# Kernel tuning notes

Measured on AMD Instinct MI355X. Metric: run time of the kernel, lower is better.

## Reference

```python
import jax, jax.numpy as jnp
import numpy as np

B = 1024          # batch
H = 1024          # rnn_num_hidden
T = 512           # max_length (encoder timesteps)
NUM = 44          # numeric features
EMB = [(30490, 64), (7, 8), (12, 8), (3, 4)]
IN = NUM + sum(d for _, d in EMB)   # input_size = 128


def lstm_cell(x, h, c, w_ih, w_hh, b_ih, b_hh):
    # PyTorch LSTM gate order: i, f, g, o
    g = x @ w_ih.T + h @ w_hh.T + b_ih + b_hh
    i, f, gg, o = jnp.split(g, 4, axis=-1)
    c2 = jax.nn.sigmoid(f) * c + jax.nn.sigmoid(i) * jnp.tanh(gg)
    h2 = jax.nn.sigmoid(o) * jnp.tanh(c2)
    return h2, c2


def setup_inputs():
    key = jax.random.key(0)
    ks = iter(jax.random.split(key, 32))
    nrm = lambda shape, s=0.02: (s * jax.random.normal(next(ks), shape)).astype(jnp.float32)
    return {
        "x": nrm((B, 1, NUM), 1.0),
        "x_emb": jax.random.randint(next(ks), (B, 1, 4), 0, 3),
        "h0": nrm((2, B, H), 1.0),
        "c0": nrm((2, B, H), 1.0),
        "encoder_outputs": nrm((T, B, H), 1.0),
        "emb0": nrm(EMB[0]), "emb1": nrm(EMB[1]), "emb2": nrm(EMB[2]), "emb3": nrm(EMB[3]),
        "attn_w": nrm((T, IN + 2 * H)), "attn_b": nrm((T,)),
        "comb_w": nrm((IN, IN + H)), "comb_b": nrm((IN,)),
        "w_ih0": nrm((4 * H, IN)), "w_hh0": nrm((4 * H, H)),
        "b_ih0": nrm((4 * H,)), "b_hh0": nrm((4 * H,)),
        "w_ih1": nrm((4 * H, H)), "w_hh1": nrm((4 * H, H)),
        "b_ih1": nrm((4 * H,)), "b_hh1": nrm((4 * H,)),
        "pred_w": nrm((1, H)), "pred_b": nrm((1,)),
    }


def reference(x, x_emb, h0, c0, encoder_outputs, emb0, emb1, emb2, emb3,
              attn_w, attn_b, comb_w, comb_b,
              w_ih0, w_hh0, b_ih0, b_hh0, w_ih1, w_hh1, b_ih1, b_hh1,
              pred_w, pred_b):
    xt = x.transpose(1, 0, 2)[0]                       # (B, NUM)
    ids = x_emb.transpose(1, 0, 2)[0]                  # (B, 4)
    e = jnp.concatenate([emb0[ids[:, 0]], emb1[ids[:, 1]],
                         emb2[ids[:, 2]], emb3[ids[:, 3]]], axis=1)
    x_rnn = jnp.concatenate([xt, e], axis=1)           # (B, IN)
    attn_in = jnp.concatenate([x_rnn, h0[0], c0[0]], axis=1)       # (B, IN+2H)
    aw = jax.nn.softmax(attn_in @ attn_w.T + attn_b, axis=1)       # (B, T)
    ctx = jnp.einsum('bt,tbh->bh', aw, encoder_outputs)            # (B, H)
    comb = jnp.concatenate([x_rnn, ctx], axis=1) @ comb_w.T + comb_b  # (B, IN)
    h1, c1 = lstm_cell(comb, h0[0], c0[0], w_ih0, w_hh0, b_ih0, b_hh0)
    h2, c2 = lstm_cell(h1, h0[1], c0[1], w_ih1, w_hh1, b_ih1, b_hh1)
    out = h2 @ pred_w.T + pred_b                       # (B, 1)
    return out, (jnp.stack([h1, h2]), jnp.stack([c1, c2])), aw
```

## Files before the change

### kernel.cpp

```cpp
#include <hip/hip_runtime.h>
#include <hip/hip_bf16.h>

#define B 1024
#define H 1024
#define T 512
#define NUM 44
#define IN 128
#define AK (IN + 2 * H)
#define G4 (4 * H)

typedef __attribute__((ext_vector_type(8))) short s16x8;
typedef __attribute__((ext_vector_type(4))) float f32x4;

__device__ __forceinline__ unsigned short f2bf(float f) {
    unsigned u = __float_as_uint(f);
    unsigned r = (u + 0x7fffu + ((u >> 16) & 1u)) >> 16;
    return (unsigned short)r;
}

__device__ __forceinline__ void gload16(const ushort* g, ushort* l) {
    __builtin_amdgcn_global_load_lds(
        (const __attribute__((address_space(1))) void*)g,
        (__attribute__((address_space(3))) void*)l,
        16, 0, 0);
}

__global__ __launch_bounds__(256) void f32_to_bf16_kernel(
    const float* __restrict__ in, ushort* __restrict__ out, int n4)
{
    int i = blockIdx.x * 256 + threadIdx.x;
    if (i >= n4) return;
    float4 v = ((const float4*)in)[i];
    ushort4 o;
    o.x = f2bf(v.x); o.y = f2bf(v.y); o.z = f2bf(v.z); o.w = f2bf(v.w);
    ((ushort4*)out)[i] = o;
}

__global__ __launch_bounds__(256) void build_attn_in_kernel(
    const float* __restrict__ x, const int* __restrict__ x_emb,
    const float* __restrict__ h0, const float* __restrict__ c0,
    const float* __restrict__ e0, const float* __restrict__ e1,
    const float* __restrict__ e2, const float* __restrict__ e3,
    ushort* __restrict__ attn_in)
{
    int b = blockIdx.x;
    int id0 = x_emb[b * 4 + 0];
    int id1 = x_emb[b * 4 + 1];
    int id2 = x_emb[b * 4 + 2];
    int id3 = x_emb[b * 4 + 3];
    ushort* dst = attn_in + (size_t)b * AK;
    for (int j = threadIdx.x; j < AK; j += 256) {
        float v;
        if (j < 44)        v = x[b * NUM + j];
        else if (j < 108)  v = e0[id0 * 64 + (j - 44)];
        else if (j < 116)  v = e1[id1 * 8 + (j - 108)];
        else if (j < 124)  v = e2[id2 * 8 + (j - 116)];
        else if (j < 128)  v = e3[id3 * 4 + (j - 124)];
        else if (j < 1152) v = h0[b * H + (j - 128)];
        else               v = c0[b * H + (j - 1152)];
        dst[j] = f2bf(v);
    }
}

#define TM 128
#define TN 128
#define TK 32

__global__ __launch_bounds__(256) void mfma_gemm_kernel(
    const ushort* __restrict__ X1, const ushort* __restrict__ W1,
    const ushort* __restrict__ X2, const ushort* __restrict__ W2,
    const float* __restrict__ bias1, const float* __restrict__ bias2,
    float* __restrict__ Cf, ushort* __restrict__ Cb,
    int K1, int ldx1, int ldw1,
    int K2, int ldx2, int ldw2,
    int N)
{
    __shared__ ushort As[TM][TK];
    __shared__ ushort Bs[TN][TK];
    const int tid = threadIdx.x;
    const int lane = tid & 63;
    const int wid = tid >> 6;
    const int wm = wid >> 1, wn = wid & 1;
    const int m0 = blockIdx.y * TM;
    const int n0 = blockIdx.x * TN;

    const int srow = wid * 32 + (lane >> 2);
    const int skc  = (lane & 3) * 8;

    f32x4 acc[4][4] = {};

    for (int phase = 0; phase < 2; ++phase) {
        const ushort* X = phase ? X2 : X1;
        const ushort* W = phase ? W2 : W1;
        const int K   = phase ? K2 : K1;
        const int ldx = phase ? ldx2 : ldx1;
        const int ldw = phase ? ldw2 : ldw1;
        if (X == nullptr || K == 0) continue;

        for (int k0 = 0; k0 < K; k0 += TK) {
            gload16(X + (size_t)(m0 + srow) * ldx + k0 + skc,      &As[wid * 32][0]);
            gload16(X + (size_t)(m0 + srow + 16) * ldx + k0 + skc, &As[wid * 32 + 16][0]);
            gload16(W + (size_t)(n0 + srow) * ldw + k0 + skc,      &Bs[wid * 32][0]);
            gload16(W + (size_t)(n0 + srow + 16) * ldw + k0 + skc, &Bs[wid * 32 + 16][0]);
            __syncthreads();

            s16x8 a[4], b[4];
            #pragma unroll
            for (int m = 0; m < 4; ++m)
                a[m] = *(const s16x8*)&As[wm * 64 + m * 16 + (lane & 15)][(lane >> 4) * 8];
            #pragma unroll
            for (int n = 0; n < 4; ++n)
                b[n] = *(const s16x8*)&Bs[wn * 64 + n * 16 + (lane & 15)][(lane >> 4) * 8];
            #pragma unroll
            for (int m = 0; m < 4; ++m)
                #pragma unroll
                for (int n = 0; n < 4; ++n)
                    acc[m][n] = __builtin_amdgcn_mfma_f32_16x16x32_bf16(a[m], b[n], acc[m][n], 0, 0, 0);
            __syncthreads();
        }
    }

    #pragma unroll
    for (int m = 0; m < 4; ++m) {
        #pragma unroll
        for (int n = 0; n < 4; ++n) {
            int col = n0 + wn * 64 + n * 16 + (lane & 15);
            float bsum = (bias1 ? bias1[col] : 0.f) + (bias2 ? bias2[col] : 0.f);
            #pragma unroll
            for (int j = 0; j < 4; ++j) {
                int row = m0 + wm * 64 + m * 16 + (lane >> 4) * 4 + j;
                float v = acc[m][n][j] + bsum;
                if (Cf) Cf[(size_t)row * N + col] = v;
                if (Cb) Cb[(size_t)row * N + col] = f2bf(v);
            }
        }
    }
}

__global__ __launch_bounds__(256) void softmax_kernel(
    const float* __restrict__ logits, float* __restrict__ aw)
{
    int b = blockIdx.x;
    const float* row = logits + (size_t)b * T;
    int tid = threadIdx.x;
    float v0 = row[tid];
    float v1 = row[tid + 256];
    float m = fmaxf(v0, v1);
    #pragma unroll
    for (int off = 32; off > 0; off >>= 1) m = fmaxf(m, __shfl_down(m, off, 64));
    __shared__ float sm[4];
    __shared__ float ss[4];
    if ((tid & 63) == 0) sm[tid >> 6] = m;
    __syncthreads();
    m = fmaxf(fmaxf(sm[0], sm[1]), fmaxf(sm[2], sm[3]));
    float e0 = expf(v0 - m), e1 = expf(v1 - m);
    float s = e0 + e1;
    #pragma unroll
    for (int off = 32; off > 0; off >>= 1) s += __shfl_down(s, off, 64);
    if ((tid & 63) == 0) ss[tid >> 6] = s;
    __syncthreads();
    s = ss[0] + ss[1] + ss[2] + ss[3];
    float inv = 1.0f / s;
    aw[(size_t)b * T + tid]       = e0 * inv;
    aw[(size_t)b * T + tid + 256] = e1 * inv;
}

__global__ __launch_bounds__(256) void ctx_kernel(
    const float* __restrict__ enc, const float* __restrict__ aw,
    ushort* __restrict__ ctx_bf)
{
    int b = blockIdx.x;
    __shared__ float w[T];
    for (int t = threadIdx.x; t < T; t += 256) w[t] = aw[(size_t)b * T + t];
    __syncthreads();
    int h0i = threadIdx.x * 4;
    const float* p = enc + (size_t)b * H + h0i;
    float4 acc = {0.f, 0.f, 0.f, 0.f};
    #pragma unroll 8
    for (int t = 0; t < T; ++t) {
        float4 v = *(const float4*)(p + (size_t)t * B * H);
        float s = w[t];
        acc.x += s * v.x; acc.y += s * v.y; acc.z += s * v.z; acc.w += s * v.w;
    }
    ushort4 o;
    o.x = f2bf(acc.x); o.y = f2bf(acc.y); o.z = f2bf(acc.z); o.w = f2bf(acc.w);
    ((ushort4*)(ctx_bf + (size_t)b * H))[threadIdx.x] = o;
}

__device__ __forceinline__ float sigmf(float v) { return 1.0f / (1.0f + expf(-v)); }

__global__ __launch_bounds__(256) void lstm_pointwise_kernel(
    const float* __restrict__ g, const float* __restrict__ c_in,
    float* __restrict__ h_out, float* __restrict__ c_out,
    ushort* __restrict__ h_bf)
{
    int idx = blockIdx.x * 256 + threadIdx.x;
    int b = idx >> 10;
    int j = idx & 1023;
    const float* gr = g + (size_t)b * G4;
    float gi = gr[j];
    float gf = gr[j + H];
    float gc = gr[j + 2 * H];
    float go = gr[j + 3 * H];
    float c = sigmf(gf) * c_in[idx] + sigmf(gi) * tanhf(gc);
    float h = sigmf(go) * tanhf(c);
    h_out[idx] = h;
    c_out[idx] = c;
    if (h_bf) h_bf[idx] = f2bf(h);
}

__global__ __launch_bounds__(256) void pred_kernel(
    const float* __restrict__ h2, const float* __restrict__ pw,
    const float* __restrict__ pb, float* __restrict__ out)
{
    int b = blockIdx.x;
    const float* row = h2 + (size_t)b * H;
    float s = 0.f;
    for (int j = threadIdx.x; j < H; j += 256) s += row[j] * pw[j];
    #pragma unroll
    for (int off = 32; off > 0; off >>= 1) s += __shfl_down(s, off, 64);
    __shared__ float sm[4];
    if ((threadIdx.x & 63) == 0) sm[threadIdx.x >> 6] = s;
    __syncthreads();
    if (threadIdx.x == 0) out[b] = sm[0] + sm[1] + sm[2] + sm[3] + pb[0];
}

extern "C" void kernel_launch(void* const* d_in, const int* in_sizes, int n_in,
                              void* d_out, int out_size, void* d_ws, size_t ws_size,
                              hipStream_t stream) {
    (void)in_sizes; (void)n_in; (void)out_size; (void)ws_size;
    const float* x      = (const float*)d_in[0];
    const int*   x_emb  = (const int*)d_in[1];
    const float* h0     = (const float*)d_in[2];
    const float* c0     = (const float*)d_in[3];
    const float* enc    = (const float*)d_in[4];
    const float* emb0   = (const float*)d_in[5];
    const float* emb1   = (const float*)d_in[6];
    const float* emb2   = (const float*)d_in[7];
    const float* emb3   = (const float*)d_in[8];
    const float* attn_w = (const float*)d_in[9];
    const float* attn_b = (const float*)d_in[10];
    const float* comb_w = (const float*)d_in[11];
    const float* comb_b = (const float*)d_in[12];
    const float* w_ih0  = (const float*)d_in[13];
    const float* w_hh0  = (const float*)d_in[14];
    const float* b_ih0  = (const float*)d_in[15];
    const float* b_hh0  = (const float*)d_in[16];
    const float* w_ih1  = (const float*)d_in[17];
    const float* w_hh1  = (const float*)d_in[18];
    const float* b_ih1  = (const float*)d_in[19];
    const float* b_hh1  = (const float*)d_in[20];
    const float* pred_w = (const float*)d_in[21];
    const float* pred_b = (const float*)d_in[22];

    float* out = (float*)d_out;
    const size_t BH = (size_t)B * H;
    float* h1_out = out + 1024;
    float* h2_out = out + 1024 + BH;
    float* c1_out = out + 1024 + 2 * BH;
    float* c2_out = out + 1024 + 3 * BH;
    float* aw_out = out + 1024 + 4 * BH;

    char* w = (char*)d_ws;
    ushort* attn_in_bf = (ushort*)w;  w += (size_t)B * AK * 2;
    ushort* h0_bf      = (ushort*)w;  w += (size_t)2 * BH * 2;
    ushort* attn_w_bf  = (ushort*)w;  w += (size_t)T * AK * 2;
    ushort* comb_w_bf  = (ushort*)w;  w += (size_t)IN * (IN + H) * 2;
    ushort* wih0_bf    = (ushort*)w;  w += (size_t)G4 * IN * 2;
    ushort* whh0_bf    = (ushort*)w;  w += (size_t)G4 * H * 2;
    ushort* wih1_bf    = (ushort*)w;  w += (size_t)G4 * H * 2;
    ushort* whh1_bf    = (ushort*)w;  w += (size_t)G4 * H * 2;
    ushort* ctx_bf     = (ushort*)w;  w += (size_t)BH * 2;
    ushort* comb_bf    = (ushort*)w;  w += (size_t)B * IN * 2;
    ushort* h1_bf      = (ushort*)w;  w += (size_t)BH * 2;
    float*  logits     = (float*)w;   w += (size_t)B * T * 4;
    float*  g          = (float*)w;   w += (size_t)B * G4 * 4;

    #define CVT(src, dst, n) f32_to_bf16_kernel<<<((n)/4 + 255)/256, 256, 0, stream>>>(src, dst, (n)/4)
    CVT(h0,     h0_bf,     2 * B * H);
    CVT(attn_w, attn_w_bf, T * AK);
    CVT(comb_w, comb_w_bf, IN * (IN + H));
    CVT(w_ih0,  wih0_bf,   G4 * IN);
    CVT(w_hh0,  whh0_bf,   G4 * H);
    CVT(w_ih1,  wih1_bf,   G4 * H);
    CVT(w_hh1,  whh1_bf,   G4 * H);
    #undef CVT

    build_attn_in_kernel<<<B, 256, 0, stream>>>(x, x_emb, h0, c0, emb0, emb1, emb2, emb3, attn_in_bf);

    mfma_gemm_kernel<<<dim3(T / TN, B / TM), 256, 0, stream>>>(
        attn_in_bf, attn_w_bf, nullptr, nullptr, attn_b, nullptr, logits, nullptr,
        AK, AK, AK, 0, 0, 0, T);

    softmax_kernel<<<B, 256, 0, stream>>>(logits, aw_out);

    ctx_kernel<<<B, 256, 0, stream>>>(enc, aw_out, ctx_bf);

    mfma_gemm_kernel<<<dim3(IN / TN, B / TM), 256, 0, stream>>>(
        attn_in_bf, comb_w_bf, ctx_bf, comb_w_bf + IN, comb_b, nullptr, nullptr, comb_bf,
        IN, AK, IN + H, H, H, IN + H, IN);

    mfma_gemm_kernel<<<dim3(G4 / TN, B / TM), 256, 0, stream>>>(
        comb_bf, wih0_bf, h0_bf, whh0_bf, b_ih0, b_hh0, g, nullptr,
        IN, IN, IN, H, H, H, G4);

    lstm_pointwise_kernel<<<(B * H) / 256, 256, 0, stream>>>(g, c0, h1_out, c1_out, h1_bf);

    mfma_gemm_kernel<<<dim3(G4 / TN, B / TM), 256, 0, stream>>>(
        h1_bf, wih1_bf, h0_bf + BH, whh1_bf, b_ih1, b_hh1, g, nullptr,
        H, H, H, H, H, H, G4);

    lstm_pointwise_kernel<<<(B * H) / 256, 256, 0, stream>>>(g, c0 + BH, h2_out, c2_out, nullptr);

    pred_kernel<<<B, 256, 0, stream>>>(h2_out, pred_w, pred_b, out);
}
```

Baseline: 671.3 us.

## Fold comb projection into LSTM weights and fuse independent stages into megakernel

Precomputes W_ih0·comb_w and a folded bias, so layer-0 gates come from one GEMM over [x_rnn, ctx] instead of a comb GEMM followed by the input GEMM. The attention logits GEMM uses split-K with partial sums reduced inside the softmax, and softmax, context reduction and both h0·W_hh GEMMs run as independent blocks of one kernel so they overlap. Weight conversions are merged into one launch. This costs an extra 4096x1152x128 weight-product GEMM per call, extra g buffers and read-modify-write epilogues, and changes the rounding order.

```diff
diff --git a/kernel.cpp b/kernel.cpp
--- a/kernel.cpp
+++ b/kernel.cpp
@@ -7,6 +7,7 @@
 #define NUM 44
 #define IN 128
 #define AK (IN + 2 * H)
+#define XC (IN + H)
 #define G4 (4 * H)
 
 typedef __attribute__((ext_vector_type(8))) short s16x8;
@@ -25,15 +26,133 @@
         16, 0, 0);
 }
 
-__global__ __launch_bounds__(256) void f32_to_bf16_kernel(
-    const float* __restrict__ in, ushort* __restrict__ out, int n4)
+#define TM 128
+#define TN 128
+#define TK 32
+
+__device__ __forceinline__ void gemm_core(
+    const ushort* __restrict__ X, const ushort* __restrict__ W,
+    const float* __restrict__ bias1, const float* __restrict__ bias2,
+    const float* __restrict__ Cin, float* __restrict__ Cf, ushort* __restrict__ Cb,
+    int kbeg, int kend, int ldx, int ldw, int ldc,
+    int m0, int n0, ushort (*As)[TK], ushort (*Bs)[TK])
+{
+    const int tid = threadIdx.x;
+    const int lane = tid & 63;
+    const int wid = tid >> 6;
+    const int wm = wid >> 1, wn = wid & 1;
+    const int srow = wid * 32 + (lane >> 2);
+    const int skc  = (lane & 3) * 8;
+
+    f32x4 acc[4][4] = {};
+
+    for (int k0 = kbeg; k0 < kend; k0 += TK) {
+        gload16(X + (size_t)(m0 + srow) * ldx + k0 + skc,      &As[wid * 32][0]);
+        gload16(X + (size_t)(m0 + srow + 16) * ldx + k0 + skc, &As[wid * 32 + 16][0]);
+        gload16(W + (size_t)(n0 + srow) * ldw + k0 + skc,      &Bs[wid * 32][0]);
+        gload16(W + (size_t)(n0 + srow + 16) * ldw + k0 + skc, &Bs[wid * 32 + 16][0]);
+        __syncthreads();
+
+        s16x8 a[4], b[4];
+        #pragma unroll
+        for (int m = 0; m < 4; ++m)
+            a[m] = *(const s16x8*)&As[wm * 64 + m * 16 + (lane & 15)][(lane >> 4) * 8];
+        #pragma unroll
+        for (int n = 0; n < 4; ++n)
+            b[n] = *(const s16x8*)&Bs[wn * 64 + n * 16 + (lane & 15)][(lane >> 4) * 8];
+        #pragma unroll
+        for (int m = 0; m < 4; ++m)
+            #pragma unroll
+            for (int n = 0; n < 4; ++n)
+                acc[m][n] = __builtin_amdgcn_mfma_f32_16x16x32_bf16(a[m], b[n], acc[m][n], 0, 0, 0);
+        __syncthreads();
+    }
+
+    #pragma unroll
+    for (int m = 0; m < 4; ++m) {
+        #pragma unroll
+        for (int n = 0; n < 4; ++n) {
+            int col = n0 + wn * 64 + n * 16 + (lane & 15);
+            float badd = (bias1 ? bias1[col] : 0.f) + (bias2 ? bias2[col] : 0.f);
+            #pragma unroll
+            for (int j = 0; j < 4; ++j) {
+                int row = m0 + wm * 64 + m * 16 + (lane >> 4) * 4 + j;
+                float v = acc[m][n][j] + badd;
+                if (Cin) v += Cin[(size_t)row * ldc + col];
+                if (Cf) Cf[(size_t)row * ldc + col] = v;
+                if (Cb) Cb[(size_t)row * ldc + col] = f2bf(v);
+            }
+        }
+    }
+}
+
+__global__ __launch_bounds__(256) void gemm_kernel(
+    const ushort* __restrict__ X, const ushort* __restrict__ W,
+    const float* __restrict__ bias1, const float* __restrict__ bias2,
+    const float* __restrict__ Cin, float* __restrict__ Cf, ushort* __restrict__ Cb,
+    int Kchunk, int ldx, int ldw, int ldc, size_t Czstride)
+{
+    __shared__ ushort As[TM][TK];
+    __shared__ ushort Bs[TN][TK];
+    int kbeg = blockIdx.z * Kchunk;
+    gemm_core(X, W, bias1, bias2, Cin,
+              Cf ? Cf + (size_t)blockIdx.z * Czstride : nullptr, Cb,
+              kbeg, kbeg + Kchunk, ldx, ldw, ldc,
+              blockIdx.y * TM, blockIdx.x * TN, As, Bs);
+}
+
+#define CN0 524288
+#define CN1 278528
+#define CN2 131072
+#define CN3 1048576
+#define CN4 1048576
+#define CN5 1048576
+#define CNT (CN0+CN1+CN2+CN3+CN4+CN5)
+
+__global__ __launch_bounds__(256) void convert_all_kernel(
+    const float* __restrict__ s0, const float* __restrict__ s1, const float* __restrict__ s2,
+    const float* __restrict__ s3, const float* __restrict__ s4, const float* __restrict__ s5,
+    ushort* __restrict__ d0, ushort* __restrict__ d1, ushort* __restrict__ d2,
+    ushort* __restrict__ d3, ushort* __restrict__ d4, ushort* __restrict__ d5)
 {
     int i = blockIdx.x * 256 + threadIdx.x;
-    if (i >= n4) return;
-    float4 v = ((const float4*)in)[i];
+    const float* s; ushort* d;
+    if (i < CN0) { s = s0; d = d0; }
+    else if ((i -= CN0) < CN1) { s = s1; d = d1; }
+    else if ((i -= CN1) < CN2) { s = s2; d = d2; }
+    else if ((i -= CN2) < CN3) { s = s3; d = d3; }
+    else if ((i -= CN3) < CN4) { s = s4; d = d4; }
+    else if ((i -= CN4) < CN5) { s = s5; d = d5; }
+    else return;
+    float4 v = ((const float4*)s)[i];
     ushort4 o;
     o.x = f2bf(v.x); o.y = f2bf(v.y); o.z = f2bf(v.z); o.w = f2bf(v.w);
-    ((ushort4*)out)[i] = o;
+    ((ushort4*)d)[i] = o;
+}
+
+__global__ __launch_bounds__(256) void transpose_combw_kernel(
+    const float* __restrict__ comb_w, ushort* __restrict__ outT)
+{
+    int idx = blockIdx.x * 256 + threadIdx.x;
+    int j = idx >> 7;
+    int k = idx & 127;
+    outT[idx] = f2bf(comb_w[(size_t)k * XC + j]);
+}
+
+__global__ __launch_bounds__(256) void bias_f_kernel(
+    const float* __restrict__ w_ih0, const float* __restrict__ comb_b,
+    const float* __restrict__ b_ih0, const float* __restrict__ b_hh0,
+    float* __restrict__ biasf)
+{
+    __shared__ float cb[IN];
+    int i = blockIdx.x * 256 + threadIdx.x;
+    for (int j = threadIdx.x; j < IN; j += 256) cb[j] = comb_b[j];
+    __syncthreads();
+    float s = b_ih0[i] + b_hh0[i];
+    const float* row = w_ih0 + (size_t)i * IN;
+    #pragma unroll 8
+    for (int j = 0; j < IN; ++j) s += row[j] * cb[j];
+    biasf[i] = s;
 }
 
 __global__ __launch_bounds__(256) void build_attn_in_kernel(
@@ -41,7 +160,7 @@
     const float* __restrict__ h0, const float* __restrict__ c0,
     const float* __restrict__ e0, const float* __restrict__ e1,
     const float* __restrict__ e2, const float* __restrict__ e3,
-    ushort* __restrict__ attn_in)
+    ushort* __restrict__ attn_in, ushort* __restrict__ xctx)
 {
     int b = blockIdx.x;
     int id0 = x_emb[b * 4 + 0];
@@ -58,133 +177,84 @@
         else if (j < 128)  v = e3[id3 * 4 + (j - 124)];
         else if (j < 1152) v = h0[b * H + (j - 128)];
         else               v = c0[b * H + (j - 1152)];
-        dst[j] = f2bf(v);
+        unsigned short bf = f2bf(v);
+        dst[j] = bf;
+        if (j < IN) xctx[(size_t)b * XC + j] = bf;
     }
 }
 
-#define TM 128
-#define TN 128
-#define TK 32
-
-__global__ __launch_bounds__(256) void mfma_gemm_kernel(
-    const ushort* __restrict__ X1, const ushort* __restrict__ W1,
-    const ushort* __restrict__ X2, const ushort* __restrict__ W2,
-    const float* __restrict__ bias1, const float* __restrict__ bias2,
-    float* __restrict__ Cf, ushort* __restrict__ Cb,
-    int K1, int ldx1, int ldw1,
-    int K2, int ldx2, int ldw2,
-    int N)
-{
-    __shared__ ushort As[TM][TK];
-    __shared__ ushort Bs[TN][TK];
-    const int tid = threadIdx.x;
-    const int lane = tid & 63;
-    const int wid = tid >> 6;
-    const int wm = wid >> 1, wn = wid & 1;
-    const int m0 = blockIdx.y * TM;
-    const int n0 = blockIdx.x * TN;
-
-    const int srow = wid * 32 + (lane >> 2);
-    const int skc  = (lane & 3) * 8;
-
-    f32x4 acc[4][4] = {};
-
-    for (int phase = 0; phase < 2; ++phase) {
-        const ushort* X = phase ? X2 : X1;
-        const ushort* W = phase ? W2 : W1;
-        const int K   = phase ? K2 : K1;
-        const int ldx = phase ? ldx2 : ldx1;
-        const int ldw = phase ? ldw2 : ldw1;
-        if (X == nullptr || K == 0) continue;
-
-        for (int k0 = 0; k0 < K; k0 += TK) {
-            gload16(X + (size_t)(m0 + srow) * ldx + k0 + skc,      &As[wid * 32][0]);
-            gload16(X + (size_t)(m0 + srow + 16) * ldx + k0 + skc, &As[wid * 32 + 16][0]);
-            gload16(W + (size_t)(n0 + srow) * ldw + k0 + skc,      &Bs[wid * 32][0]);
-            gload16(W + (size_t)(n0 + srow + 16) * ldw + k0 + skc, &Bs[wid * 32 + 16][0]);
-            __syncthreads();
-
-            s16x8 a[4], b[4];
-            #pragma unroll
-            for (int m = 0; m < 4; ++m)
-                a[m] = *(const s16x8*)&As[wm * 64 + m * 16 + (lane & 15)][(lane >> 4) * 8];
-            #pragma unroll
-            for (int n = 0; n < 4; ++n)
-                b[n] = *(const s16x8*)&Bs[wn * 64 + n * 16 + (lane & 15)][(lane >> 4) * 8];
-            #pragma unroll
-            for (int m = 0; m < 4; ++m)
-                #pragma unroll
-                for (int n = 0; n < 4; ++n)
-                    acc[m][n] = __builtin_amdgcn_mfma_f32_16x16x32_bf16(a[m], b[n], acc[m][n], 0, 0, 0);
-            __syncthreads();
+__global__ __launch_bounds__(256) void mega_kernel(
+    const ushort* __restrict__ h0_bf, const ushort* __restrict__ whh0_bf,
+    const ushort* __restrict__ whh1_bf, float* __restrict__ g1buf, float* __restrict__ g2buf,
+    const ushort* __restrict__ wih0_bf, const ushort* __restrict__ comb_wT_bf,
+    ushort* __restrict__ W_f_bf,
+    const float* __restrict__ logits_part, const float* __restrict__ attn_b,
+    float* __restrict__ aw_out, const float* __restrict__ enc, ushort* __restrict__ xctx)
+{
+    __shared__ union {
+        struct { ushort As[TM][TK]; ushort Bs[TN][TK]; } g;
+        struct { float w[T]; float red[8]; } c;
+    } sh;
+
+    const int bid = blockIdx.x;
+    if (bid < 512) {
+        int layer = bid >> 8;
+        int t = bid & 255;
+        int m0 = (t >> 5) * TM;
+        int n0 = (t & 31) * TN;
+        gemm_core(h0_bf + (size_t)layer * B * H, layer ? whh1_bf : whh0_bf,
+                  nullptr, nullptr, nullptr, layer ? g2buf : g1buf, nullptr,
+                  0, H, H, H, G4, m0, n0, sh.g.As, sh.g.Bs);
+    } else if (bid < 800) {
+        int t = bid - 512;
+        int m0 = (t / 9) * TM;
+        int n0 = (t % 9) * TN;
+        gemm_core(wih0_bf, comb_wT_bf, nullptr, nullptr, nullptr, nullptr, W_f_bf,
+                  0, IN, IN, IN, XC, m0, n0, sh.g.As, sh.g.Bs);
+    } else {
+        int b = bid - 800;
+        int tid = threadIdx.x;
+        float v0 = attn_b[tid], v1 = attn_b[tid + 256];
+        #pragma unroll
+        for (int z = 0; z < 4; ++z) {
+            const float* lp = logits_part + (size_t)z * B * T + (size_t)b * T;
+            v0 += lp[tid];
+            v1 += lp[tid + 256];
         }
+        float m = fmaxf(v0, v1);
+        #pragma unroll
+        for (int off = 32; off > 0; off >>= 1) m = fmaxf(m, __shfl_down(m, off, 64));
+        if ((tid & 63) == 0) sh.c.red[tid >> 6] = m;
+        __syncthreads();
+        m = fmaxf(fmaxf(sh.c.red[0], sh.c.red[1]), fmaxf(sh.c.red[2], sh.c.red[3]));
+        float e0 = expf(v0 - m), e1 = expf(v1 - m);
+        float s = e0 + e1;
+        #pragma unroll
+        for (int off = 32; off > 0; off >>= 1) s += __shfl_down(s, off, 64);
+        if ((tid & 63) == 0) sh.c.red[4 + (tid >> 6)] = s;
+        __syncthreads();
+        s = sh.c.red[4] + sh.c.red[5] + sh.c.red[6] + sh.c.red[7];
+        float inv = 1.0f / s;
+        float w0 = e0 * inv, w1 = e1 * inv;
+        sh.c.w[tid] = w0;
+        sh.c.w[tid + 256] = w1;
+        aw_out[(size_t)b * T + tid]       = w0;
+        aw_out[(size_t)b * T + tid + 256] = w1;
+        __syncthreads();
+
+        int h0i = tid * 4;
+        const float* p = enc + (size_t)b * H + h0i;
+        float4 acc = {0.f, 0.f, 0.f, 0.f};
+        #pragma unroll 8
+        for (int t = 0; t < T; ++t) {
+            float4 v = *(const float4*)(p + (size_t)t * B * H);
+            float sw = sh.c.w[t];
+            acc.x += sw * v.x; acc.y += sw * v.y; acc.z += sw * v.z; acc.w += sw * v.w;
+        }
+        ushort4 o;
+        o.x = f2bf(acc.x); o.y = f2bf(acc.y); o.z = f2bf(acc.z); o.w = f2bf(acc.w);
+        *(ushort4*)(xctx + (size_t)b * XC + IN + h0i) = o;
     }
-
-    #pragma unroll
-    for (int m = 0; m < 4; ++m) {
-        #pragma unroll
-        for (int n = 0; n < 4; ++n) {
-            int col = n0 + wn * 64 + n * 16 + (lane & 15);
-            float bsum = (bias1 ? bias1[col] : 0.f) + (bias2 ? bias2[col] : 0.f);
-            #pragma unroll
-            for (int j = 0; j < 4; ++j) {
-                int row = m0 + wm * 64 + m * 16 + (lane >> 4) * 4 + j;
-                float v = acc[m][n][j] + bsum;
-                if (Cf) Cf[(size_t)row * N + col] = v;
-                if (Cb) Cb[(size_t)row * N + col] = f2bf(v);
-            }
-        }
-    }
-}
-
-__global__ __launch_bounds__(256) void softmax_kernel(
-    const float* __restrict__ logits, float* __restrict__ aw)
-{
-    int b = blockIdx.x;
-    const float* row = logits + (size_t)b * T;
-    int tid = threadIdx.x;
-    float v0 = row[tid];
-    float v1 = row[tid + 256];
-    float m = fmaxf(v0, v1);
-    #pragma unroll
-    for (int off = 32; off > 0; off >>= 1) m = fmaxf(m, __shfl_down(m, off, 64));
-    __shared__ float sm[4];
-    __shared__ float ss[4];
-    if ((tid & 63) == 0) sm[tid >> 6] = m;
-    __syncthreads();
-    m = fmaxf(fmaxf(sm[0], sm[1]), fmaxf(sm[2], sm[3]));
-    float e0 = expf(v0 - m), e1 = expf(v1 - m);
-    float s = e0 + e1;
-    #pragma unroll
-    for (int off = 32; off > 0; off >>= 1) s += __shfl_down(s, off, 64);
-    if ((tid & 63) == 0) ss[tid >> 6] = s;
-    __syncthreads();
-    s = ss[0] + ss[1] + ss[2] + ss[3];
-    float inv = 1.0f / s;
-    aw[(size_t)b * T + tid]       = e0 * inv;
-    aw[(size_t)b * T + tid + 256] = e1 * inv;
-}
-
-__global__ __launch_bounds__(256) void ctx_kernel(
-    const float* __restrict__ enc, const float* __restrict__ aw,
-    ushort* __restrict__ ctx_bf)
-{
-    int b = blockIdx.x;
-    __shared__ float w[T];
-    for (int t = threadIdx.x; t < T; t += 256) w[t] = aw[(size_t)b * T + t];
-    __syncthreads();
-    int h0i = threadIdx.x * 4;
-    const float* p = enc + (size_t)b * H + h0i;
-    float4 acc = {0.f, 0.f, 0.f, 0.f};
-    #pragma unroll 8
-    for (int t = 0; t < T; ++t) {
-        float4 v = *(const float4*)(p + (size_t)t * B * H);
-        float s = w[t];
-        acc.x += s * v.x; acc.y += s * v.y; acc.z += s * v.z; acc.w += s * v.w;
-    }
-    ushort4 o;
-    o.x = f2bf(acc.x); o.y = f2bf(acc.y); o.z = f2bf(acc.z); o.w = f2bf(acc.w);
-    ((ushort4*)(ctx_bf + (size_t)b * H))[threadIdx.x] = o;
 }
 
 __device__ __forceinline__ float sigmf(float v) { return 1.0f / (1.0f + expf(-v)); }
@@ -265,52 +335,50 @@
     ushort* attn_in_bf = (ushort*)w;  w += (size_t)B * AK * 2;
     ushort* h0_bf      = (ushort*)w;  w += (size_t)2 * BH * 2;
     ushort* attn_w_bf  = (ushort*)w;  w += (size_t)T * AK * 2;
-    ushort* comb_w_bf  = (ushort*)w;  w += (size_t)IN * (IN + H) * 2;
     ushort* wih0_bf    = (ushort*)w;  w += (size_t)G4 * IN * 2;
     ushort* whh0_bf    = (ushort*)w;  w += (size_t)G4 * H * 2;
     ushort* wih1_bf    = (ushort*)w;  w += (size_t)G4 * H * 2;
     ushort* whh1_bf    = (ushort*)w;  w += (size_t)G4 * H * 2;
-    ushort* ctx_bf     = (ushort*)w;  w += (size_t)BH * 2;
-    ushort* comb_bf    = (ushort*)w;  w += (size_t)B * IN * 2;
+    ushort* comb_wT_bf = (ushort*)w;  w += (size_t)XC * IN * 2;
+    ushort* W_f_bf     = (ushort*)w;  w += (size_t)G4 * XC * 2;
+    float*  bias_f     = (float*)w;   w += (size_t)G4 * 4;
+    ushort* xctx_bf    = (ushort*)w;  w += (size_t)B * XC * 2;
     ushort* h1_bf      = (ushort*)w;  w += (size_t)BH * 2;
-    float*  logits     = (float*)w;   w += (size_t)B * T * 4;
-    float*  g          = (float*)w;   w += (size_t)B * G4 * 4;
-
-    #define CVT(src, dst, n) f32_to_bf16_kernel<<<((n)/4 + 255)/256, 256, 0, stream>>>(src, dst, (n)/4)
-    CVT(h0,     h0_bf,     2 * B * H);
-    CVT(attn_w, attn_w_bf, T * AK);
-    CVT(comb_w, comb_w_bf, IN * (IN + H));
-    CVT(w_ih0,  wih0_bf,   G4 * IN);
-    CVT(w_hh0,  whh0_bf,   G4 * H);
-    CVT(w_ih1,  wih1_bf,   G4 * H);
-    CVT(w_hh1,  whh1_bf,   G4 * H);
-    #undef CVT
-
-    build_attn_in_kernel<<<B, 256, 0, stream>>>(x, x_emb, h0, c0, emb0, emb1, emb2, emb3, attn_in_bf);
-
-    mfma_gemm_kernel<<<dim3(T / TN, B / TM), 256, 0, stream>>>(
-        attn_in_bf, attn_w_bf, nullptr, nullptr, attn_b, nullptr, logits, nullptr,
-        AK, AK, AK, 0, 0, 0, T);
-
-    softmax_kernel<<<B, 256, 0, stream>>>(logits, aw_out);
-
-    ctx_kernel<<<B, 256, 0, stream>>>(enc, aw_out, ctx_bf);
-
-    mfma_gemm_kernel<<<dim3(IN / TN, B / TM), 256, 0, stream>>>(
-        attn_in_bf, comb_w_bf, ctx_bf, comb_w_bf + IN, comb_b, nullptr, nullptr, comb_bf,
-        IN, AK, IN + H, H, H, IN + H, IN);
-
-    mfma_gemm_kernel<<<dim3(G4 / TN, B / TM), 256, 0, stream>>>(
-        comb_bf, wih0_bf, h0_bf, whh0_bf, b_ih0, b_hh0, g, nullptr,
-        IN, IN, IN, H, H, H, G4);
-
-    lstm_pointwise_kernel<<<(B * H) / 256, 256, 0, stream>>>(g, c0, h1_out, c1_out, h1_bf);
-
-    mfma_gemm_kernel<<<dim3(G4 / TN, B / TM), 256, 0, stream>>>(
-        h1_bf, wih1_bf, h0_bf + BH, whh1_bf, b_ih1, b_hh1, g, nullptr,
-        H, H, H, H, H, H, G4);
-
-    lstm_pointwise_kernel<<<(B * H) / 256, 256, 0, stream>>>(g, c0 + BH, h2_out, c2_out, nullptr);
+    float*  logits_p   = (float*)w;   w += (size_t)4 * B * T * 4;
+    float*  g1buf      = (float*)w;   w += (size_t)B * G4 * 4;
+    float*  g2buf      = (float*)w;   w += (size_t)B * G4 * 4;
+
+    convert_all_kernel<<<(CNT + 255) / 256, 256, 0, stream>>>(
+        h0, attn_w, w_ih0, w_hh0, w_ih1, w_hh1,
+        h0_bf, attn_w_bf, wih0_bf, whh0_bf, wih1_bf, whh1_bf);
+
+    transpose_combw_kernel<<<(XC * IN) / 256, 256, 0, stream>>>(comb_w, comb_wT_bf);
+
+    bias_f_kernel<<<G4 / 256, 256, 0, stream>>>(w_ih0, comb_b, b_ih0, b_hh0, bias_f);
+
+    build_attn_in_kernel<<<B, 256, 0, stream>>>(x, x_emb, h0, c0, emb0, emb1, emb2, emb3,
+                                                attn_in_bf, xctx_bf);
+
+    gemm_kernel<<<dim3(T / TN, B / TM, 4), 256, 0, stream>>>(
+        attn_in_bf, attn_w_bf, nullptr, nullptr, nullptr, logits_p, nullptr,
+        544, AK, AK, T, (size_t)B * T);
+
+    mega_kernel<<<1824, 256, 0, stream>>>(
+        h0_bf, whh0_bf, whh1_bf, g1buf, g2buf,
+        wih0_bf, comb_wT_bf, W_f_bf,
+        logits_p, attn_b, aw_out, enc, xctx_bf);
+
+    gemm_kernel<<<dim3(G4 / TN, B / TM, 1), 256, 0, stream>>>(
+        xctx_bf, W_f_bf, bias_f, nullptr, g1buf, g1buf, nullptr,
+        XC, XC, XC, G4, 0);
+
+    lstm_pointwise_kernel<<<(B * H) / 256, 256, 0, stream>>>(g1buf, c0, h1_out, c1_out, h1_bf);
+
+    gemm_kernel<<<dim3(G4 / TN, B / TM, 1), 256, 0, stream>>>(
+        h1_bf, wih1_bf, b_ih1, b_hh1, g2buf, g2buf, nullptr,
+        H, H, H, G4, 0);
+
+    lstm_pointwise_kernel<<<(B * H) / 256, 256, 0, stream>>>(g2buf, c0 + BH, h2_out, c2_out, nullptr);
 
     pred_kernel<<<B, 256, 0, stream>>>(h2_out, pred_w, pred_b, out);
 }
```

Result: faster. 644.4 us (-4.0%).
